# Optimization experiments

Hardware: AMD Instinct MI355X
Metric: run time of the kernel (lower is better)

Reference implementation:

```python
import jax, jax.numpy as jnp
import numpy as np

EPS = 1e-7  # K.epsilon()
N_ROUTINGS = 3


def squash(v, axis=-1):
    s2 = jnp.sum(jnp.square(v), axis=axis, keepdims=True)
    scale = s2 / (1.0 + s2) / jnp.sqrt(s2 + EPS)
    return scale * v


def setup_inputs() -> dict:
    key = jax.random.key(0)
    k1, k2 = jax.random.split(key)
    B, IN_CAPS, IN_DIM = 128, 1152, 8
    N_CAPS, DIM = 32, 16
    inputs = jax.random.normal(k1, (B, IN_CAPS, IN_DIM), dtype=jnp.float32)
    # glorot-uniform-ish scale for W [n_capsule, in_caps, dim_capsule, in_dim]
    limit = np.sqrt(6.0 / (IN_DIM + DIM)).astype(np.float32)
    W = jax.random.uniform(k2, (N_CAPS, IN_CAPS, DIM, IN_DIM), dtype=jnp.float32,
                           minval=-limit, maxval=limit)
    return {"inputs": inputs, "W": W}


def reference(inputs, W):
    # inputs: [b, i, l]; W: [j, i, k, l] -> u_hat: [b, j, i, k]
    u_hat = jnp.einsum('jikl,bil->bjik', W, inputs)
    b = jnp.zeros(u_hat.shape[:3], dtype=u_hat.dtype)  # [b, j, i]
    v = None
    for r in range(N_ROUTINGS):
        c = jax.nn.softmax(b, axis=1)                 # softmax over output caps j
        s = jnp.einsum('bji,bjik->bjk', c, u_hat)     # weighted sum over input caps i
        v = squash(s, axis=-1)                        # [b, j, k]
        if r < N_ROUTINGS - 1:
            b = b + jnp.einsum('bjik,bjk->bji', u_hat, v)  # agreement
    return v
```

## Files before the change

### kernel.cpp

```cpp
#include <hip/hip_runtime.h>
#include <hip/hip_bf16.h>
#include <stdint.h>


using fab = __attribute__((ext_vector_type(8))) short;
using fcc = __attribute__((ext_vector_type(4))) float;

__device__ __forceinline__ uint32_t bfr(float f) {
    uint32_t u = __float_as_uint(f);
    return (u + 0x7fffu + ((u >> 16) & 1u)) >> 16;
}

__global__ __launch_bounds__(256)
void prep(const float* __restrict__ W, const float* __restrict__ x,
          ushort* __restrict__ W3, ushort* __restrict__ X2)
{
    const int t = blockIdx.x * 256 + threadIdx.x;
    {
        const int k = t & 15, j = (t >> 4) & 31, i = t >> 9;
        const float* src = W + (((size_t)j * 1152 + i) * 16 + k) * 8;
        const float4 a = *reinterpret_cast<const float4*>(src);
        const float4 b = *reinterpret_cast<const float4*>(src + 4);
        uint4 o;
        o.x = bfr(a.x) | (bfr(a.y) << 16);
        o.y = bfr(a.z) | (bfr(a.w) << 16);
        o.z = bfr(b.x) | (bfr(b.y) << 16);
        o.w = bfr(b.z) | (bfr(b.w) << 16);
        *reinterpret_cast<uint4*>(W3 + (size_t)t * 8) = o;
    }
    if (t < 147456) {
        const int b = t & 127, i = t >> 7;
        const float* src = x + ((size_t)b * 1152 + i) * 8;
        const float4 a = *reinterpret_cast<const float4*>(src);
        const float4 bb = *reinterpret_cast<const float4*>(src + 4);
        uint4 o;
        o.x = bfr(a.x) | (bfr(a.y) << 16);
        o.y = bfr(a.z) | (bfr(a.w) << 16);
        o.z = bfr(bb.x) | (bfr(bb.y) << 16);
        o.w = bfr(bb.z) | (bfr(bb.w) << 16);
        *reinterpret_cast<uint4*>(X2 + (size_t)t * 8) = o;
    }
}

template<int R>
__global__ __launch_bounds__(512)
void caps_route_mfma(const ushort* __restrict__ W3,
                     const ushort* __restrict__ X2,
                     const float* __restrict__ s0,
                     const float* __restrict__ s1,
                     float* __restrict__ sout)
{
    __shared__ float pl[2][8][16];
    __shared__ float tr[8][1024];

    const int tid  = threadIdx.x;
    const int lane = tid & 63;
    const int w    = tid >> 6;
    const int bl   = lane & 15;
    const int kg   = lane >> 4;
    const bool lo  = (kg == 0);
    const int bg   = blockIdx.x >> 6;
    const int sl   = blockIdx.x & 63;
    const int i0   = sl * 18;
    const int b0   = bg * 16;

    fab zf;
    #pragma unroll
    for (int q = 0; q < 8; ++q) zf[q] = 0;

    auto loadA = [&](int i, int t) -> fab {
        return lo ? *reinterpret_cast<const fab*>(
                        W3 + (((size_t)i * 32 + w * 4 + t) * 16 + bl) * 8)
                  : zf;
    };
    auto loadB = [&](int i) -> fab {
        return lo ? *reinterpret_cast<const fab*>(
                        X2 + ((size_t)i * 128 + b0 + bl) * 8)
                  : zf;
    };

    float Vr[4][4];
    if (R > 0) {
        #pragma unroll
        for (int t = 0; t < 4; ++t) {
            const size_t ro = ((size_t)(b0 + bl) * 32 + w * 4 + t) * 16 + kg * 4;
            const float4 a = *reinterpret_cast<const float4*>(s0 + ro);
            float q = a.x * a.x + a.y * a.y + a.z * a.z + a.w * a.w;
            q += __shfl_xor(q, 16);
            q += __shfl_xor(q, 32);
            const float sc = q / ((1.0f + q) * sqrtf(q + 1e-7f)) * 1.44269504f;
            Vr[t][0] = a.x * sc; Vr[t][1] = a.y * sc;
            Vr[t][2] = a.z * sc; Vr[t][3] = a.w * sc;
            if (R == 2) {
                const float4 b = *reinterpret_cast<const float4*>(s1 + ro);
                float q1 = b.x * b.x + b.y * b.y + b.z * b.z + b.w * b.w;
                q1 += __shfl_xor(q1, 16);
                q1 += __shfl_xor(q1, 32);
                const float sc1 =
                    q1 / ((1.0f + q1) * sqrtf(q1 + 1e-7f)) * 1.44269504f;
                Vr[t][0] += b.x * sc1; Vr[t][1] += b.y * sc1;
                Vr[t][2] += b.z * sc1; Vr[t][3] += b.w * sc1;
            }
        }
    }

    fcc sacc[4];
    #pragma unroll
    for (int t = 0; t < 4; ++t)
        #pragma unroll
        for (int r = 0; r < 4; ++r) sacc[t][r] = 0.0f;

    auto body = [&](const fab* A, const fab& B, int ii) {
        const fcc cz = {0.0f, 0.0f, 0.0f, 0.0f};
        fcc u[4];
        #pragma unroll
        for (int t = 0; t < 4; ++t)
            u[t] = __builtin_amdgcn_mfma_f32_16x16x32_bf16(A[t], B, cz, 0, 0, 0);

        float cf4[4];
        if (R == 0) {
            #pragma unroll
            for (int t = 0; t < 4; ++t) cf4[t] = 0.03125f;
        } else {
            float e[4];
            float ps = 0.0f;
            #pragma unroll
            for (int t = 0; t < 4; ++t) {
                float p = u[t][0] * Vr[t][0];
                p = fmaf(u[t][1], Vr[t][1], p);
                p = fmaf(u[t][2], Vr[t][2], p);
                p = fmaf(u[t][3], Vr[t][3], p);
                p += __shfl_xor(p, 16);
                p += __shfl_xor(p, 32);
                e[t] = exp2f(p);
                ps += e[t];
            }
            const int ib = ii & 1;
            if (lane < 16) pl[ib][w][bl] = ps;
            __syncthreads();
            float den = pl[ib][0][bl];
            #pragma unroll
            for (int ww = 1; ww < 8; ++ww) den += pl[ib][ww][bl];
            const float inv = __builtin_amdgcn_rcpf(den);
            #pragma unroll
            for (int t = 0; t < 4; ++t) cf4[t] = e[t] * inv;
        }
        #pragma unroll
        for (int t = 0; t < 4; ++t)
            #pragma unroll
            for (int r = 0; r < 4; ++r)
                sacc[t][r] = fmaf(cf4[t], u[t][r], sacc[t][r]);
    };

    fab A0[4], A1[4], B0, B1;
    #pragma unroll
    for (int t = 0; t < 4; ++t) A0[t] = loadA(i0, t);
    B0 = loadB(i0);

    for (int ii = 0; ii < 18; ii += 2) {
        {
            const int ip = i0 + ii + 1;
            #pragma unroll
            for (int t = 0; t < 4; ++t) A1[t] = loadA(ip, t);
            B1 = loadB(ip);
        }
        body(A0, B0, ii);
        {
            int ip = i0 + ii + 2;
            if (ip > 1151) ip = 1151;
            #pragma unroll
            for (int t = 0; t < 4; ++t) A0[t] = loadA(ip, t);
            B0 = loadB(ip);
        }
        body(A1, B1, ii + 1);
    }

    {
        float* ep = &tr[w][0];
        #pragma unroll
        for (int t = 0; t < 4; ++t)
            #pragma unroll
            for (int r = 0; r < 4; ++r) {
                const int off = t * 16 + kg * 4 + r;
                ep[off * 16 + (bl ^ (off & 15))] = sacc[t][r];
            }
        float* sg = sout + (size_t)b0 * 512 + w * 64;
        #pragma unroll
        for (int c = 0; c < 16; ++c) {
            const float v = ep[lane * 16 + (c ^ (lane & 15))];
            atomicAdd(&sg[(size_t)c * 512 + lane], v);
        }
    }
}

__global__ __launch_bounds__(256)
void caps_squash_out(const float* __restrict__ s2, float* __restrict__ out)
{
    const int t = blockIdx.x * 256 + threadIdx.x;
    const float sv = s2[t];
    float p = sv * sv;
    p += __shfl_xor(p, 1);
    p += __shfl_xor(p, 2);
    p += __shfl_xor(p, 4);
    p += __shfl_xor(p, 8);
    const float scale = p / ((1.0f + p) * sqrtf(p + 1e-7f));
    out[t] = scale * sv;
}

#define WJ        (1152 * 128)
#define I_TILE_F  24
#define NSLICE_F  48

template<int R>
__global__ __launch_bounds__(256)
void caps_route_f32(const float* __restrict__ x,
                    const float* __restrict__ W,
                    const float* __restrict__ Vacc,
                    float* __restrict__ s)
{
    __shared__ float Wt[2][4096];
    __shared__ float xs[8 * 192];

    const int tid  = threadIdx.x;
    const int lane = tid & 63;
    const int wv   = tid >> 6;
    const int j    = lane & 31;
    const int kh   = lane >> 5;
    const int bg   = blockIdx.x / NSLICE_F;
    const int sl   = blockIdx.x % NSLICE_F;
    const int i0   = sl * I_TILE_F;
    const int b0   = bg * 8 + wv * 2;

    const float* wsrc[4];
    #pragma unroll
    for (int t = 0; t < 4; ++t) {
        const int q  = (wv * 4 + t) * 1024 + lane * 16;
        const int rr = q >> 8;
        const int cb = (q & 255) ^ ((rr & 15) << 4);
        const int js = rr & 31;
        const int c  = (rr >> 5) * 64 + (cb >> 2);
        wsrc[t] = W + (size_t)js * WJ + c;
    }

    auto stage = [&](int buf, int i) {
        #pragma unroll
        for (int t = 0; t < 4; ++t)
            __builtin_amdgcn_global_load_lds(
                (const __attribute__((address_space(1))) uint32_t*)
                    (wsrc[t] + (size_t)i * 128),
                (__attribute__((address_space(3))) uint32_t*)
                    &Wt[buf][(wv * 4 + t) * 256], 16, 0, 0);
    };

    stage(0, i0);

    for (int cf = tid; cf < 384; cf += 256) {
        const int bl = cf / 48;
        const int rm = cf - bl * 48;
        float4 v = *reinterpret_cast<const float4*>(
            x + ((size_t)(bg * 8 + bl) * 1152 + i0) * 8 + rm * 4);
        *reinterpret_cast<float4*>(xs + bl * 192 + rm * 4) = v;
    }

    float Vr[2][8];
    if (R > 0) {
        #pragma unroll
        for (int bb = 0; bb < 2; ++bb) {
            const float* vp = Vacc + ((size_t)(b0 + bb) * 32 + j) * 16 + kh * 8;
            const float4 va = *reinterpret_cast<const float4*>(vp);
            const float4 vb = *reinterpret_cast<const float4*>(vp + 4);
            Vr[bb][0] = va.x * 1.44269504f; Vr[bb][1] = va.y * 1.44269504f;
            Vr[bb][2] = va.z * 1.44269504f; Vr[bb][3] = va.w * 1.44269504f;
            Vr[bb][4] = vb.x * 1.44269504f; Vr[bb][5] = vb.y * 1.44269504f;
            Vr[bb][6] = vb.z * 1.44269504f; Vr[bb][7] = vb.w * 1.44269504f;
        }
    }

    float sacc[2][8];
    #pragma unroll
    for (int bb = 0; bb < 2; ++bb)
        #pragma unroll
        for (int kk = 0; kk < 8; ++kk) sacc[bb][kk] = 0.0f;

    __syncthreads();

    const int sw = (j & 15) << 4;

    for (int ii = 0; ii < I_TILE_F; ++ii) {
        const int cur = ii & 1;
        if (ii + 1 < I_TILE_F) stage(cur ^ 1, i0 + ii + 1);

        float4 xa[2], xb[2];
        #pragma unroll
        for (int bb = 0; bb < 2; ++bb) {
            const float* xp = xs + (wv * 2 + bb) * 192 + ii * 8;
            xa[bb] = *reinterpret_cast<const float4*>(xp);
            xb[bb] = *reinterpret_cast<const float4*>(xp + 4);
        }

        const char* lbase = reinterpret_cast<const char*>(&Wt[cur][0]) + lane * 256;

        float u[2][8];
        #pragma unroll
        for (int kk = 0; kk < 8; ++kk) {
            const float4 w0 = *reinterpret_cast<const float4*>(lbase + ((kk * 32) ^ sw));
            const float4 w1 = *reinterpret_cast<const float4*>(lbase + ((kk * 32 + 16) ^ sw));
            #pragma unroll
            for (int bb = 0; bb < 2; ++bb) {
                float acc;
                acc = w0.x * xa[bb].x;
                acc = fmaf(w0.y, xa[bb].y, acc);
                acc = fmaf(w0.z, xa[bb].z, acc);
                acc = fmaf(w0.w, xa[bb].w, acc);
                acc = fmaf(w1.x, xb[bb].x, acc);
                acc = fmaf(w1.y, xb[bb].y, acc);
                acc = fmaf(w1.z, xb[bb].z, acc);
                acc = fmaf(w1.w, xb[bb].w, acc);
                u[bb][kk] = acc;
            }
        }

        if (R == 0) {
            #pragma unroll
            for (int bb = 0; bb < 2; ++bb)
                #pragma unroll
                for (int kk = 0; kk < 8; ++kk)
                    sacc[bb][kk] = fmaf(0.03125f, u[bb][kk], sacc[bb][kk]);
        } else {
            float p0 = u[0][0] * Vr[0][0];
            float p1 = u[1][0] * Vr[1][0];
            #pragma unroll
            for (int kk = 1; kk < 8; ++kk) {
                p0 = fmaf(u[0][kk], Vr[0][kk], p0);
                p1 = fmaf(u[1][kk], Vr[1][kk], p1);
            }
            p0 += __shfl_xor(p0, 32);
            p1 += __shfl_xor(p1, 32);
            const float pq = kh ? p1 : p0;
            const float e  = exp2f(pq);
            float den = e;
            den += __shfl_xor(den, 1);
            den += __shfl_xor(den, 2);
            den += __shfl_xor(den, 4);
            den += __shfl_xor(den, 8);
            den += __shfl_xor(den, 16);
            const float cf_own = e * __builtin_amdgcn_rcpf(den);
            const float cf_oth = __shfl_xor(cf_own, 32);
            const float cf0 = kh ? cf_oth : cf_own;
            const float cf1 = kh ? cf_own : cf_oth;
            #pragma unroll
            for (int kk = 0; kk < 8; ++kk) {
                sacc[0][kk] = fmaf(cf0, u[0][kk], sacc[0][kk]);
                sacc[1][kk] = fmaf(cf1, u[1][kk], sacc[1][kk]);
            }
        }
        __syncthreads();
    }

    {
        float* ep = &Wt[0][0] + wv * 1024;
        #pragma unroll
        for (int bb = 0; bb < 2; ++bb)
            #pragma unroll
            for (int kk = 0; kk < 8; ++kk)
                ep[bb * 512 + j * 16 + ((kh * 8 + kk) ^ ((j >> 1) & 15))] =
                    sacc[bb][kk];

        float* sg = s + (size_t)b0 * 512;
        #pragma unroll
        for (int c = 0; c < 16; ++c) {
            const int m   = c * 64 + lane;
            const int bb2 = m >> 9;
            const int j2  = (m >> 4) & 31;
            const int k2  = m & 15;
            const float v = ep[bb2 * 512 + j2 * 16 + (k2 ^ ((j2 >> 1) & 15))];
            atomicAdd(&sg[m], v);
        }
    }
}

template<int MODE>
__global__ __launch_bounds__(256)
void caps_squash(float* __restrict__ s,
                 float* __restrict__ Vacc,
                 float* __restrict__ out)
{
    const int t = blockIdx.x * 256 + threadIdx.x;
    const float sv = s[t];
    float p = sv * sv;
    p += __shfl_xor(p, 1);
    p += __shfl_xor(p, 2);
    p += __shfl_xor(p, 4);
    p += __shfl_xor(p, 8);
    const float scale = p / ((1.0f + p) * sqrtf(p + 1e-7f));
    const float v = scale * sv;
    if (MODE == 0)      { Vacc[t] = v;  s[t] = 0.0f; }
    else if (MODE == 1) { Vacc[t] += v; s[t] = 0.0f; }
    else                { out[t] = v; }
}

extern "C" void kernel_launch(void* const* d_in, const int* in_sizes, int n_in,
                              void* d_out, int out_size, void* d_ws, size_t ws_size,
                              hipStream_t stream)
{
    const float* x = (const float*)d_in[0];
    const float* W = (const float*)d_in[1];
    float* out = (float*)d_out;

    const size_t W3B = (size_t)589824 * 16;
    const size_t X2B = (size_t)147456 * 16;
    const size_t SB  = (size_t)65536 * sizeof(float);

    if (ws_size >= W3B + X2B + 3 * SB) {
        ushort* W3 = (ushort*)d_ws;
        ushort* X2 = (ushort*)((char*)d_ws + W3B);
        float* s0  = (float*)((char*)d_ws + W3B + X2B);
        float* s1  = s0 + 65536;
        float* s2  = s1 + 65536;

        hipMemsetAsync(s0, 0, 3 * SB, stream);
        prep<<<2304, 256, 0, stream>>>(W, x, W3, X2);

        dim3 grid(512);
        dim3 blk(512);
        caps_route_mfma<0><<<grid, blk, 0, stream>>>(W3, X2, s0, s0, s0);
        caps_route_mfma<1><<<grid, blk, 0, stream>>>(W3, X2, s0, s0, s1);
        caps_route_mfma<2><<<grid, blk, 0, stream>>>(W3, X2, s0, s1, s2);
        caps_squash_out<<<256, 256, 0, stream>>>(s2, out);
    } else {
        float* Vacc = (float*)d_ws;
        float* sbuf = Vacc + 65536;
        hipMemsetAsync(sbuf, 0, SB, stream);

        dim3 grid(16 * NSLICE_F);
        dim3 blk(256);
        caps_route_f32<0><<<grid, blk, 0, stream>>>(x, W, Vacc, sbuf);
        caps_squash<0><<<256, 256, 0, stream>>>(sbuf, Vacc, out);
        caps_route_f32<1><<<grid, blk, 0, stream>>>(x, W, Vacc, sbuf);
        caps_squash<1><<<256, 256, 0, stream>>>(sbuf, Vacc, out);
        caps_route_f32<2><<<grid, blk, 0, stream>>>(x, W, Vacc, sbuf);
        caps_squash<2><<<256, 256, 0, stream>>>(sbuf, Vacc, out);
    }
}
```

Before: 114.4 us.

## Pack K dimension in first routing pass and halve softmax barriers

Adds a dedicated first-iteration kernel that spreads four input capsules across the lane groups of each MFMA's K dimension. The MFMA result accumulates the uniform-coefficient sum directly, so the kernel needs about a quarter as many MFMA instructions and no per-capsule softmax. The later routing kernels now compute softmax partials for two input capsules before one shared __syncthreads, halving the block-wide barriers. They also add a launch_bounds occupancy hint. The cost is more register pressure from keeping two u tiles live, plus a padded shared-memory layout for the partial sums.

```diff
diff --git a/kernel.cpp b/kernel.cpp
--- a/kernel.cpp
+++ b/kernel.cpp
@@ -42,15 +42,94 @@
     }
 }
 
+__global__ __launch_bounds__(512)
+void caps_route0(const ushort* __restrict__ W3,
+                 const ushort* __restrict__ X2,
+                 float* __restrict__ sout)
+{
+    __shared__ float tr[8][1024];
+
+    const int tid  = threadIdx.x;
+    const int lane = tid & 63;
+    const int w    = tid >> 6;
+    const int bl   = lane & 15;
+    const int kg   = lane >> 4;
+    const int bg   = blockIdx.x >> 6;
+    const int sl   = blockIdx.x & 63;
+    const int i0   = sl * 18;
+    const int b0   = bg * 16;
+
+    fab zf;
+    #pragma unroll
+    for (int q = 0; q < 8; ++q) zf[q] = 0;
+
+    auto loadAq = [&](int g, int t, bool ok) -> fab {
+        return ok ? *reinterpret_cast<const fab*>(
+                       W3 + (((size_t)(i0 + 4 * g + kg) * 32 + w * 4 + t) * 16 + bl) * 8)
+                  : zf;
+    };
+    auto loadBq = [&](int g, bool ok) -> fab {
+        return ok ? *reinterpret_cast<const fab*>(
+                       X2 + ((size_t)(i0 + 4 * g + kg) * 128 + b0 + bl) * 8)
+                  : zf;
+    };
+
+    fcc sacc[4];
+    #pragma unroll
+    for (int t = 0; t < 4; ++t)
+        #pragma unroll
+        for (int r = 0; r < 4; ++r) sacc[t][r] = 0.0f;
+
+    fab Ac[4], An[4], Bc, Bn;
+    #pragma unroll
+    for (int t = 0; t < 4; ++t) Ac[t] = loadAq(0, t, true);
+    Bc = loadBq(0, true);
+
+    #pragma unroll
+    for (int g = 0; g < 5; ++g) {
+        if (g < 4) {
+            const bool ok = (g + 1 < 4) | (kg < 2);
+            #pragma unroll
+            for (int t = 0; t < 4; ++t) An[t] = loadAq(g + 1, t, ok);
+            Bn = loadBq(g + 1, ok);
+        }
+        #pragma unroll
+        for (int t = 0; t < 4; ++t)
+            sacc[t] = __builtin_amdgcn_mfma_f32_16x16x32_bf16(Ac[t], Bc, sacc[t], 0, 0, 0);
+        if (g < 4) {
+            #pragma unroll
+            for (int t = 0; t < 4; ++t) Ac[t] = An[t];
+            Bc = Bn;
+        }
+    }
+
+    {
+        float* ep = &tr[w][0];
+        #pragma unroll
+        for (int t = 0; t < 4; ++t)
+            #pragma unroll
+            for (int r = 0; r < 4; ++r) {
+                const int off = t * 16 + kg * 4 + r;
+                ep[off * 16 + (bl ^ (off & 15))] = sacc[t][r] * 0.03125f;
+            }
+        float* sg = sout + (size_t)b0 * 512 + w * 64;
+        #pragma unroll
+        for (int c = 0; c < 16; ++c) {
+            const float v = ep[lane * 16 + (c ^ (lane & 15))];
+            atomicAdd(&sg[(size_t)c * 512 + lane], v);
+        }
+    }
+}
+
 template<int R>
-__global__ __launch_bounds__(512)
-void caps_route_mfma(const ushort* __restrict__ W3,
-                     const ushort* __restrict__ X2,
-                     const float* __restrict__ s0,
-                     const float* __restrict__ s1,
-                     float* __restrict__ sout)
-{
-    __shared__ float pl[2][8][16];
+__global__ __launch_bounds__(512, 4)
+void caps_route_sm(const ushort* __restrict__ W3,
+                   const ushort* __restrict__ X2,
+                   const float* __restrict__ s0,
+                   const float* __restrict__ s1,
+                   float* __restrict__ sout)
+{
+    __shared__ float pl[2][8][16][2];
     __shared__ float tr[8][1024];
 
     const int tid  = threadIdx.x;
@@ -80,27 +159,24 @@
     };
 
     float Vr[4][4];
-    if (R > 0) {
-        #pragma unroll
-        for (int t = 0; t < 4; ++t) {
-            const size_t ro = ((size_t)(b0 + bl) * 32 + w * 4 + t) * 16 + kg * 4;
-            const float4 a = *reinterpret_cast<const float4*>(s0 + ro);
-            float q = a.x * a.x + a.y * a.y + a.z * a.z + a.w * a.w;
-            q += __shfl_xor(q, 16);
-            q += __shfl_xor(q, 32);
-            const float sc = q / ((1.0f + q) * sqrtf(q + 1e-7f)) * 1.44269504f;
-            Vr[t][0] = a.x * sc; Vr[t][1] = a.y * sc;
-            Vr[t][2] = a.z * sc; Vr[t][3] = a.w * sc;
-            if (R == 2) {
-                const float4 b = *reinterpret_cast<const float4*>(s1 + ro);
-                float q1 = b.x * b.x + b.y * b.y + b.z * b.z + b.w * b.w;
-                q1 += __shfl_xor(q1, 16);
-                q1 += __shfl_xor(q1, 32);
-                const float sc1 =
-                    q1 / ((1.0f + q1) * sqrtf(q1 + 1e-7f)) * 1.44269504f;
-                Vr[t][0] += b.x * sc1; Vr[t][1] += b.y * sc1;
-                Vr[t][2] += b.z * sc1; Vr[t][3] += b.w * sc1;
-            }
+    #pragma unroll
+    for (int t = 0; t < 4; ++t) {
+        const size_t ro = ((size_t)(b0 + bl) * 32 + w * 4 + t) * 16 + kg * 4;
+        const float4 a = *reinterpret_cast<const float4*>(s0 + ro);
+        float q = a.x * a.x + a.y * a.y + a.z * a.z + a.w * a.w;
+        q += __shfl_xor(q, 16);
+        q += __shfl_xor(q, 32);
+        const float sc = q / ((1.0f + q) * sqrtf(q + 1e-7f)) * 1.44269504f;
+        Vr[t][0] = a.x * sc; Vr[t][1] = a.y * sc;
+        Vr[t][2] = a.z * sc; Vr[t][3] = a.w * sc;
+        if (R == 2) {
+            const float4 b = *reinterpret_cast<const float4*>(s1 + ro);
+            float q1 = b.x * b.x + b.y * b.y + b.z * b.z + b.w * b.w;
+            q1 += __shfl_xor(q1, 16);
+            q1 += __shfl_xor(q1, 32);
+            const float sc1 = q1 / ((1.0f + q1) * sqrtf(q1 + 1e-7f)) * 1.44269504f;
+            Vr[t][0] += b.x * sc1; Vr[t][1] += b.y * sc1;
+            Vr[t][2] += b.z * sc1; Vr[t][3] += b.w * sc1;
         }
     }
 
@@ -110,69 +186,82 @@
         #pragma unroll
         for (int r = 0; r < 4; ++r) sacc[t][r] = 0.0f;
 
-    auto body = [&](const fab* A, const fab& B, int ii) {
-        const fcc cz = {0.0f, 0.0f, 0.0f, 0.0f};
-        fcc u[4];
-        #pragma unroll
-        for (int t = 0; t < 4; ++t)
-            u[t] = __builtin_amdgcn_mfma_f32_16x16x32_bf16(A[t], B, cz, 0, 0, 0);
-
-        float cf4[4];
-        if (R == 0) {
-            #pragma unroll
-            for (int t = 0; t < 4; ++t) cf4[t] = 0.03125f;
-        } else {
-            float e[4];
-            float ps = 0.0f;
-            #pragma unroll
-            for (int t = 0; t < 4; ++t) {
-                float p = u[t][0] * Vr[t][0];
-                p = fmaf(u[t][1], Vr[t][1], p);
-                p = fmaf(u[t][2], Vr[t][2], p);
-                p = fmaf(u[t][3], Vr[t][3], p);
-                p += __shfl_xor(p, 16);
-                p += __shfl_xor(p, 32);
-                e[t] = exp2f(p);
-                ps += e[t];
-            }
-            const int ib = ii & 1;
-            if (lane < 16) pl[ib][w][bl] = ps;
-            __syncthreads();
-            float den = pl[ib][0][bl];
-            #pragma unroll
-            for (int ww = 1; ww < 8; ++ww) den += pl[ib][ww][bl];
-            const float inv = __builtin_amdgcn_rcpf(den);
-            #pragma unroll
-            for (int t = 0; t < 4; ++t) cf4[t] = e[t] * inv;
-        }
-        #pragma unroll
-        for (int t = 0; t < 4; ++t)
-            #pragma unroll
-            for (int r = 0; r < 4; ++r)
-                sacc[t][r] = fmaf(cf4[t], u[t][r], sacc[t][r]);
-    };
+    const fcc cz = {0.0f, 0.0f, 0.0f, 0.0f};
 
     fab A0[4], A1[4], B0, B1;
     #pragma unroll
     for (int t = 0; t < 4; ++t) A0[t] = loadA(i0, t);
     B0 = loadB(i0);
 
-    for (int ii = 0; ii < 18; ii += 2) {
-        {
-            const int ip = i0 + ii + 1;
-            #pragma unroll
-            for (int t = 0; t < 4; ++t) A1[t] = loadA(ip, t);
-            B1 = loadB(ip);
-        }
-        body(A0, B0, ii);
-        {
-            int ip = i0 + ii + 2;
-            if (ip > 1151) ip = 1151;
-            #pragma unroll
-            for (int t = 0; t < 4; ++t) A0[t] = loadA(ip, t);
-            B0 = loadB(ip);
-        }
-        body(A1, B1, ii + 1);
+    for (int pp = 0; pp < 9; ++pp) {
+        const int ie = i0 + 2 * pp;
+        #pragma unroll
+        for (int t = 0; t < 4; ++t) A1[t] = loadA(ie + 1, t);
+        B1 = loadB(ie + 1);
+
+        fcc ue[4];
+        #pragma unroll
+        for (int t = 0; t < 4; ++t)
+            ue[t] = __builtin_amdgcn_mfma_f32_16x16x32_bf16(A0[t], B0, cz, 0, 0, 0);
+        float ee[4], pse = 0.0f;
+        #pragma unroll
+        for (int t = 0; t < 4; ++t) {
+            float p = ue[t][0] * Vr[t][0];
+            p = fmaf(ue[t][1], Vr[t][1], p);
+            p = fmaf(ue[t][2], Vr[t][2], p);
+            p = fmaf(ue[t][3], Vr[t][3], p);
+            p += __shfl_xor(p, 16);
+            p += __shfl_xor(p, 32);
+            ee[t] = exp2f(p);
+            pse += ee[t];
+        }
+        if (lane < 16) pl[pp & 1][w][bl][0] = pse;
+
+        if (pp < 8) {
+            #pragma unroll
+            for (int t = 0; t < 4; ++t) A0[t] = loadA(ie + 2, t);
+            B0 = loadB(ie + 2);
+        }
+
+        fcc uo[4];
+        #pragma unroll
+        for (int t = 0; t < 4; ++t)
+            uo[t] = __builtin_amdgcn_mfma_f32_16x16x32_bf16(A1[t], B1, cz, 0, 0, 0);
+        float eo[4], pso = 0.0f;
+        #pragma unroll
+        for (int t = 0; t < 4; ++t) {
+            float p = uo[t][0] * Vr[t][0];
+            p = fmaf(uo[t][1], Vr[t][1], p);
+            p = fmaf(uo[t][2], Vr[t][2], p);
+            p = fmaf(uo[t][3], Vr[t][3], p);
+            p += __shfl_xor(p, 16);
+            p += __shfl_xor(p, 32);
+            eo[t] = exp2f(p);
+            pso += eo[t];
+        }
+        if (lane >= 16 && lane < 32) pl[pp & 1][w][bl][1] = pso;
+
+        __syncthreads();
+
+        float dene = 0.0f, deno = 0.0f;
+        #pragma unroll
+        for (int ww = 0; ww < 8; ++ww) {
+            const float2 d = *reinterpret_cast<const float2*>(&pl[pp & 1][ww][bl][0]);
+            dene += d.x;
+            deno += d.y;
+        }
+        const float inve = __builtin_amdgcn_rcpf(dene);
+        const float invo = __builtin_amdgcn_rcpf(deno);
+        #pragma unroll
+        for (int t = 0; t < 4; ++t) {
+            const float cfe = ee[t] * inve;
+            const float cfo = eo[t] * invo;
+            #pragma unroll
+            for (int r = 0; r < 4; ++r) {
+                sacc[t][r] = fmaf(cfe, ue[t][r], sacc[t][r]);
+                sacc[t][r] = fmaf(cfo, uo[t][r], sacc[t][r]);
+            }
+        }
     }
 
     {
@@ -423,9 +512,9 @@
 
         dim3 grid(512);
         dim3 blk(512);
-        caps_route_mfma<0><<<grid, blk, 0, stream>>>(W3, X2, s0, s0, s0);
-        caps_route_mfma<1><<<grid, blk, 0, stream>>>(W3, X2, s0, s0, s1);
-        caps_route_mfma<2><<<grid, blk, 0, stream>>>(W3, X2, s0, s1, s2);
+        caps_route0<<<grid, blk, 0, stream>>>(W3, X2, s0);
+        caps_route_sm<1><<<grid, blk, 0, stream>>>(W3, X2, s0, s0, s1);
+        caps_route_sm<2><<<grid, blk, 0, stream>>>(W3, X2, s0, s1, s2);
         caps_squash_out<<<256, 256, 0, stream>>>(s2, out);
     } else {
         float* Vacc = (float*)d_ws;
```

Result: faster. 105.7 us (-7.6%).
